# Kernel tuning notes

Measured on AMD Instinct MI355X. Metric: run time of the kernel, lower is better.

Reference implementation:

```python
import jax, jax.numpy as jnp
import numpy as np

B, N, D = 2, 2048, 256
H = 8
HD = D // H
SCALE = HD ** 0.5  # NOTE: source MULTIPLIES by sqrt(head_dim)
EPS = 1e-5
DFF = 4 * D


def setup_inputs() -> dict:
    key = jax.random.key(0)
    ks = jax.random.split(key, 9)
    s = lambda fan_in: 1.0 / np.sqrt(fan_in)
    return {
        "x": jax.random.normal(ks[0], (B, N, D), dtype=jnp.float32),
        # weights stored [in, out] (transposed torch Linear)
        "qkv_w": jax.random.normal(ks[1], (D, 3 * D), dtype=jnp.float32) * s(D),
        "proj_w": jax.random.normal(ks[2], (D, D), dtype=jnp.float32) * s(D),
        "proj_b": jax.random.normal(ks[3], (D,), dtype=jnp.float32) * 0.01,
        "fc1_w": jax.random.normal(ks[4], (D, DFF), dtype=jnp.float32) * s(D),
        "fc1_b": jax.random.normal(ks[5], (DFF,), dtype=jnp.float32) * 0.01,
        "fc2_w": jax.random.normal(ks[6], (DFF, D), dtype=jnp.float32) * s(DFF),
        "fc2_b": jax.random.normal(ks[7], (D,), dtype=jnp.float32) * 0.01,
        "ln1_g": jnp.ones((D,), dtype=jnp.float32),
        "ln1_b": jnp.zeros((D,), dtype=jnp.float32),
    }


def _layernorm(x, g, b):
    mu = jnp.mean(x, axis=-1, keepdims=True)
    var = jnp.mean(jnp.square(x - mu), axis=-1, keepdims=True)
    return (x - mu) * jax.lax.rsqrt(var + EPS) * g + b


def reference(x, qkv_w, proj_w, proj_b, fc1_w, fc1_b, fc2_w, fc2_b, ln1_g, ln1_b):
    b, n, d = x.shape
    # --- MHA ---
    qkv = (x @ qkv_w).reshape(b, n, 3, H, HD)
    q = qkv[:, :, 0].transpose(0, 2, 1, 3)  # [B,H,N,HD]
    k = qkv[:, :, 1].transpose(0, 2, 1, 3)
    v = qkv[:, :, 2].transpose(0, 2, 1, 3)
    att = jnp.einsum("bhqd,bhkd->bhqk", q, k) * SCALE  # multiplied, per source
    att = jax.nn.softmax(att, axis=-1)
    out = jnp.einsum("bhqk,bhkd->bhqd", att, v)
    out = out.transpose(0, 2, 1, 3).reshape(b, n, d)
    out = out @ proj_w + proj_b
    # --- post-norm residual ---
    net = _layernorm(out + x, ln1_g, ln1_b)
    shortcut = net
    # --- MLP (NO activation in source forward) ---
    net = (net @ fc1_w + fc1_b) @ fc2_w + fc2_b
    return net + shortcut
```

## Files before the change

### kernel.cpp

```cpp
#include <hip/hip_runtime.h>


typedef __attribute__((ext_vector_type(8))) short short8;
typedef __attribute__((ext_vector_type(4))) short bf16x4;
typedef __attribute__((ext_vector_type(4))) float floatx4;
typedef unsigned short u16;

#define MFMA32(a,b,c) __builtin_amdgcn_mfma_f32_16x16x32_bf16((a),(b),(c),0,0,0)
#if __has_builtin(__builtin_amdgcn_mfma_f32_16x16x16_bf16)
#define MFMAPV(a,b,c) __builtin_amdgcn_mfma_f32_16x16x16_bf16((a),(b),(c),0,0,0)
#else
#define MFMAPV(a,b,c) __builtin_amdgcn_mfma_f32_16x16x16bf16_1k((a),(b),(c),0,0,0)
#endif
#define CLF 8.1615404f

__device__ __forceinline__ float bf2f(u16 u) { return __uint_as_float(((unsigned)u) << 16); }
__device__ __forceinline__ u16 f2bf(float f) {
  unsigned u = __float_as_uint(f);
  u += 0x7fffu + ((u >> 16) & 1u);
  return (u16)(u >> 16);
}
__device__ __forceinline__ void gll16(const void* g, void* l) {
  __builtin_amdgcn_global_load_lds((const __attribute__((address_space(1))) void*)g,
                                   (__attribute__((address_space(3))) void*)l, 16, 0, 0);
}

__global__ __launch_bounds__(256) void prep_k(
    const void* __restrict__ x, const void* __restrict__ qkv_w,
    const void* __restrict__ proj_w, const void* __restrict__ fc1_w,
    const void* __restrict__ fc2_w, const void* __restrict__ proj_b,
    const void* __restrict__ fc1_b, const void* __restrict__ fc2_b,
    const void* __restrict__ ln_g, const void* __restrict__ ln_b,
    u16* __restrict__ x_hi, u16* __restrict__ x_lo,
    u16* __restrict__ wq_hi, u16* __restrict__ wq_lo,
    u16* __restrict__ wt_proj, u16* __restrict__ wt_fc1, u16* __restrict__ wt_fc2,
    u16* __restrict__ b_proj, u16* __restrict__ b_fc1, u16* __restrict__ b_fc2,
    u16* __restrict__ g_ln, u16* __restrict__ bb_ln)
{
  const int lane = threadIdx.x & 63;
  const float probe = bf2f(((const u16*)qkv_w)[lane]);
  const bool f32 = __ballot(!(fabsf(probe) < 1000.0f)) != 0ull;
  const int bid = blockIdx.x, tid = threadIdx.x;
  #define RD(p, i) (f32 ? ((const float*)(p))[i] : bf2f(((const u16*)(p))[i]))
  if (bid < 4096) {
    const size_t i = (size_t)bid * 256 + tid;
    const float f = RD(x, i); const u16 h = f2bf(f);
    x_hi[i] = h; x_lo[i] = f2bf(f - bf2f(h));
  } else if (bid < 4864) {
    const int idx = (bid - 4096) * 256 + tid;
    const int n = idx >> 8, k = idx & 255;
    const float f = RD(qkv_w, (size_t)k * 768 + n); const u16 h = f2bf(f);
    wq_hi[idx] = h; wq_lo[idx] = f2bf(f - bf2f(h));
  } else if (bid < 5120) {
    const int idx = (bid - 4864) * 256 + tid;
    wt_proj[idx] = f2bf(RD(proj_w, (size_t)(idx & 255) * 256 + (idx >> 8)));
  } else if (bid < 6144) {
    const int idx = (bid - 5120) * 256 + tid;
    wt_fc1[idx] = f2bf(RD(fc1_w, (size_t)(idx & 255) * 1024 + (idx >> 8)));
  } else if (bid < 7168) {
    const int idx = (bid - 6144) * 256 + tid;
    wt_fc2[idx] = f2bf(RD(fc2_w, (size_t)(idx & 1023) * 256 + (idx >> 10)));
  } else {
    const int j = (bid - 7168) * 256 + tid;
    if (j < 256)       b_proj[j]        = f2bf(RD(proj_b, j));
    else if (j < 1280) b_fc1[j - 256]   = f2bf(RD(fc1_b, j - 256));
    else if (j < 1536) b_fc2[j - 1280]  = f2bf(RD(fc2_b, j - 1280));
    else if (j < 1792) g_ln[j - 1536]   = f2bf(RD(ln_g, j - 1536));
    else               bb_ln[j - 1792]  = f2bf(RD(ln_b, j - 1792));
  }
  #undef RD
}

template<int TW, int EPI, bool BIAS, bool RES, bool SPLIT>
__global__ __launch_bounds__(256) void gemm_k(
    const u16* __restrict__ A, const u16* __restrict__ Bt,
    const u16* __restrict__ A2, const u16* __restrict__ B2,
    const u16* __restrict__ bias, const u16* __restrict__ res,
    void* __restrict__ out0, u16* __restrict__ aux1, u16* __restrict__ aux2,
    u16* __restrict__ aux3, u16* __restrict__ aux4,
    int M, int Nn, int K)
{
  constexpr int BT = TW * 32;
  constexpr int NC = (TW > 1 ? TW / 2 : 1);
  __shared__ __align__(16) short As[BT][40];
  __shared__ __align__(16) short Bs[BT][40];
  __shared__ __align__(16) short As2[SPLIT ? BT : 1][40];
  __shared__ __align__(16) short Bs2[SPLIT ? BT : 1][40];
  const int tid = threadIdx.x;
  const int m0 = blockIdx.y * BT, n0 = blockIdx.x * BT;
  const bool sp = SPLIT && (n0 < 512);
  const int wid = tid >> 6, lane = tid & 63;
  const int wm = (wid >> 1) * (TW * 16), wn = (wid & 1) * (TW * 16);
  const int lm = lane & 15, quad = lane >> 4;

  floatx4 zero = {0.f, 0.f, 0.f, 0.f};
  floatx4 acc[TW][TW];
#pragma unroll
  for (int i = 0; i < TW; ++i)
#pragma unroll
    for (int j = 0; j < TW; ++j) acc[i][j] = zero;

  int srow[NC], soff[NC];
  short8 ra[NC], rb[NC], ra2[NC], rb2[NC];
#pragma unroll
  for (int c = 0; c < NC; ++c) {
    const int cid = tid * NC + c;
    srow[c] = cid >> 2; soff[c] = (cid & 3) * 8;
  }
#pragma unroll
  for (int c = 0; c < NC; ++c) {
    const size_t ga = (size_t)(m0 + srow[c]) * K + soff[c];
    const size_t gb = (size_t)(n0 + srow[c]) * K + soff[c];
    ra[c] = *(const short8*)&A[ga];  rb[c] = *(const short8*)&Bt[gb];
    if (sp) { ra2[c] = *(const short8*)&A2[ga]; rb2[c] = *(const short8*)&B2[gb]; }
  }

  for (int k0 = 0; k0 < K; k0 += 32) {
    if (k0) __syncthreads();
#pragma unroll
    for (int c = 0; c < NC; ++c) {
      *(short8*)&As[srow[c]][soff[c]] = ra[c];
      *(short8*)&Bs[srow[c]][soff[c]] = rb[c];
      if (sp) {
        *(short8*)&As2[srow[c]][soff[c]] = ra2[c];
        *(short8*)&Bs2[srow[c]][soff[c]] = rb2[c];
      }
    }
    __syncthreads();
    if (k0 + 32 < K) {
#pragma unroll
      for (int c = 0; c < NC; ++c) {
        const size_t ga = (size_t)(m0 + srow[c]) * K + k0 + 32 + soff[c];
        const size_t gb = (size_t)(n0 + srow[c]) * K + k0 + 32 + soff[c];
        ra[c] = *(const short8*)&A[ga];  rb[c] = *(const short8*)&Bt[gb];
        if (sp) { ra2[c] = *(const short8*)&A2[ga]; rb2[c] = *(const short8*)&B2[gb]; }
      }
    }
    short8 fa[TW], fb[TW], fa2[TW], fb2[TW];
#pragma unroll
    for (int t = 0; t < TW; ++t) {
      fa[t] = *(const short8*)&As[wm + t * 16 + lm][quad * 8];
      fb[t] = *(const short8*)&Bs[wn + t * 16 + lm][quad * 8];
      if (sp) {
        fa2[t] = *(const short8*)&As2[wm + t * 16 + lm][quad * 8];
        fb2[t] = *(const short8*)&Bs2[wn + t * 16 + lm][quad * 8];
      }
    }
#pragma unroll
    for (int i = 0; i < TW; ++i)
#pragma unroll
      for (int j = 0; j < TW; ++j) {
        if (sp) {
          acc[i][j] = MFMA32(fa[i], fb2[j], acc[i][j]);
          acc[i][j] = MFMA32(fa2[i], fb[j], acc[i][j]);
        }
        acc[i][j] = MFMA32(fa[i], fb[j], acc[i][j]);
      }
  }

#pragma unroll
  for (int i = 0; i < TW; ++i) {
    const int rowb = m0 + wm + i * 16 + quad * 4;
#pragma unroll
    for (int j = 0; j < TW; ++j) {
      const int col = n0 + wn + j * 16 + lm;
      const float bv = BIAS ? bf2f(bias[col]) : 0.f;
#pragma unroll
      for (int r = 0; r < 4; ++r) {
        const int row = rowb + r;
        float v = acc[i][j][r] + bv;
        const size_t o = (size_t)row * Nn + col;
        if (RES) v += bf2f(res[o]);
        if (EPI == 0) {
          ((float*)out0)[o] = v;
        } else if (EPI == 1) {
          ((u16*)out0)[o] = f2bf(v);
        } else {
          u16 hi = f2bf(v);
          u16 lo = f2bf(v - bf2f(hi));
          if (col < 256) {
            const size_t oq = (size_t)row * 256 + col;
            aux1[oq] = hi; aux2[oq] = lo;
          } else if (col < 512) {
            const size_t ok = (size_t)row * 256 + (col - 256);
            aux3[ok] = hi; aux4[ok] = lo;
          } else {
            int d = col & 31, hh = (col >> 5) & 7;
            int bb = row >> 11, n = row & 2047;
            ((u16*)out0)[(size_t)((bb * 8 + hh) * 32 + d) * 2048 + n] = hi;
          }
        }
      }
    }
  }
}

template<int CHUNKS>
__global__ __launch_bounds__(256) void attn_k(
    const u16* __restrict__ qhi, const u16* __restrict__ qlo,
    const u16* __restrict__ khi, const u16* __restrict__ klo,
    const u16* __restrict__ vt, u16* __restrict__ outp, u16* __restrict__ out23,
    float* __restrict__ mu)
{
  __shared__ __align__(16) u16 Khi[2][64][32];
  __shared__ __align__(16) u16 Klo[2][64][32];
  __shared__ __align__(16) u16 Vs [2][32][64];
  const int tid = threadIdx.x, wid = tid >> 6, lane = tid & 63;
  const int lm = lane & 15, quad = lane >> 4;
  const int bid = blockIdx.x;
  const int chunk = (CHUNKS > 1) ? (bid >> 9) : 0;
  const int qblk = bid & 31, bh = (bid >> 5) & 15;
  const int b = bh >> 3, h = bh & 7;
  const int q0 = qblk * 64 + wid * 16;
  const size_t tb = (size_t)b * 2048;
  const int NT = 32 / CHUNKS;
  const int kofs = chunk * (2048 / CHUNKS);

  short8 qh, ql;
  { size_t off = (tb + q0 + lm) * 256 + h * 32 + quad * 8;
    qh = *(const short8*)&qhi[off];
    ql = *(const short8*)&qlo[off]; }

  const int kkey = tid >> 2, kg = tid & 3;
  const size_t kb = (tb + kofs + kkey) * 256 + h * 32 + kg * 8;
  const int vd = tid >> 3, vp = tid & 7, vk8 = vp ^ (vd & 7);
  const size_t vb = (size_t)(bh * 32 + vd) * 2048 + kofs + vk8 * 8;

  gll16(khi + kb, (u16*)Khi + tid * 8);
  gll16(klo + kb, (u16*)Klo + tid * 8);
  gll16(vt  + vb, (u16*)Vs  + tid * 8);

  float mrun = -1e30f, lrun = 0.f;
  floatx4 o0 = {0.f,0.f,0.f,0.f}, o1 = {0.f,0.f,0.f,0.f};

  for (int kt = 0; kt < NT; ++kt) {
    const int buf = kt & 1;
    __syncthreads();
    if (kt < NT - 1) {
      const int nb = (buf ^ 1) * 2048;
      const size_t ko = (size_t)(kt + 1) * 16384;
      const size_t vo = (size_t)(kt + 1) * 64;
      gll16(khi + kb + ko, (u16*)Khi + nb + tid * 8);
      gll16(klo + kb + ko, (u16*)Klo + nb + tid * 8);
      gll16(vt  + vb + vo, (u16*)Vs  + nb + tid * 8);
    }

    floatx4 z[4];
#pragma unroll
    for (int kf = 0; kf < 4; ++kf) {
      short8 khf = *(const short8*)&Khi[buf][kf * 16 + lm][quad * 8];
      short8 klf = *(const short8*)&Klo[buf][kf * 16 + lm][quad * 8];
      floatx4 zz = {0.f,0.f,0.f,0.f};
      zz = MFMA32(khf, ql, zz);
      zz = MFMA32(klf, qh, zz);
      zz = MFMA32(khf, qh, zz);
      z[kf] = zz;
    }
    float zm = fmaxf(fmaxf(fmaxf(z[0][0], z[0][1]), fmaxf(z[0][2], z[0][3])),
               fmaxf(fmaxf(z[1][0], z[1][1]), fmaxf(z[1][2], z[1][3])));
    zm = fmaxf(zm, fmaxf(fmaxf(fmaxf(z[2][0], z[2][1]), fmaxf(z[2][2], z[2][3])),
                   fmaxf(fmaxf(z[3][0], z[3][1]), fmaxf(z[3][2], z[3][3]))));
    zm = fmaxf(zm, __shfl_xor(zm, 16));
    zm = fmaxf(zm, __shfl_xor(zm, 32));
    const float mn = fmaxf(mrun, zm);
    const float alpha = exp2f((mrun - mn) * CLF);
    const float mc = mn * CLF;
    mrun = mn;
    float ls = 0.f;
    bf16x4 pb[4];
#pragma unroll
    for (int kf = 0; kf < 4; ++kf)
#pragma unroll
      for (int r = 0; r < 4; ++r) {
        const float p = exp2f(__builtin_fmaf(z[kf][r], CLF, -mc));
        ls += p;
        pb[kf][r] = (short)f2bf(p);
      }
    ls += __shfl_xor(ls, 16);
    ls += __shfl_xor(ls, 32);
    lrun = lrun * alpha + ls;
#pragma unroll
    for (int r = 0; r < 4; ++r) { o0[r] *= alpha; o1[r] *= alpha; }
    const u16* vbase = (const u16*)Vs + buf * 2048;
#pragma unroll
    for (int kf = 0; kf < 4; ++kf) {
      const int k8 = 2 * kf + (quad >> 1);
      const int d0 = lm, d1 = 16 + lm;
      bf16x4 vf0 = *(const bf16x4*)(vbase + (d0 * 8 + (k8 ^ (d0 & 7))) * 8 + (quad & 1) * 4);
      bf16x4 vf1 = *(const bf16x4*)(vbase + (d1 * 8 + (k8 ^ (d1 & 7))) * 8 + (quad & 1) * 4);
      o0 = MFMAPV(vf0, pb[kf], o0);
      o1 = MFMAPV(vf1, pb[kf], o1);
    }
  }
  const float inv = 1.0f / lrun;
  const size_t tok = tb + q0 + lm;
  u16* dst = ((CHUNKS > 2 && chunk >= 2) ? out23 : outp) + (size_t)(chunk & 1) * 1048576;
  const size_t rowo = tok * 256 + h * 32;
#pragma unroll
  for (int r = 0; r < 4; ++r) {
    dst[rowo + quad * 4 + r]      = f2bf(o0[r] * inv);
    dst[rowo + 16 + quad * 4 + r] = f2bf(o1[r] * inv);
  }
  if (CHUNKS > 1 && quad == 0)
    mu[chunk * 32768 + tok * 8 + h] = __builtin_fmaf(mrun, CLF, __log2f(lrun));
}

template<int CHUNKS>
__global__ __launch_bounds__(256) void combine_k(u16* __restrict__ d,
                                                 const u16* __restrict__ e,
                                                 const float* __restrict__ mu)
{
  const int t = blockIdx.x, c = threadIdx.x, h = c >> 5;
  const size_t o = (size_t)t * 256 + c;
  float m[CHUNKS];
  float M = -1e30f;
#pragma unroll
  for (int i = 0; i < CHUNKS; ++i) { m[i] = mu[i * 32768 + t * 8 + h]; M = fmaxf(M, m[i]); }
  float wsum = 0.f, acc = 0.f;
#pragma unroll
  for (int i = 0; i < CHUNKS; ++i) {
    const float w = exp2f(m[i] - M);
    const u16 v = (i < 2) ? d[o + (size_t)i * 1048576] : e[o + (size_t)(i - 2) * 1048576];
    wsum += w; acc += w * bf2f(v);
  }
  d[o] = f2bf(acc / wsum);
}

__global__ __launch_bounds__(256) void ln_k(const float* __restrict__ pf,
                                            const u16* __restrict__ xh,
                                            const u16* __restrict__ xl,
                                            const u16* __restrict__ g,
                                            const u16* __restrict__ bta,
                                            u16* __restrict__ net)
{
  const int t = blockIdx.x, c = threadIdx.x;
  const size_t o = (size_t)t * 256 + c;
  float v = pf[o] + bf2f(xh[o]) + bf2f(xl[o]);
  float s = v, s2 = v * v;
#pragma unroll
  for (int d = 1; d < 64; d <<= 1) { s += __shfl_xor(s, d); s2 += __shfl_xor(s2, d); }
  __shared__ float ss[4], ss2[4];
  const int w = c >> 6;
  if ((c & 63) == 0) { ss[w] = s; ss2[w] = s2; }
  __syncthreads();
  s = ss[0] + ss[1] + ss[2] + ss[3];
  s2 = ss2[0] + ss2[1] + ss2[2] + ss2[3];
  const float mu = s * (1.f / 256.f);
  const float var = s2 * (1.f / 256.f) - mu * mu;
  const float is = rsqrtf(var + 1e-5f);
  net[o] = f2bf((v - mu) * is * bf2f(g[c]) + bf2f(bta[c]));
}

extern "C" void kernel_launch(void* const* d_in, const int* in_sizes, int n_in,
                              void* d_out, int out_size, void* d_ws, size_t ws_size,
                              hipStream_t stream) {
  const void* x      = d_in[0];
  const void* qkv_w  = d_in[1];
  const void* proj_w = d_in[2];
  const void* proj_b = d_in[3];
  const void* fc1_w  = d_in[4];
  const void* fc1_b  = d_in[5];
  const void* fc2_w  = d_in[6];
  const void* fc2_b  = d_in[7];
  const void* ln_g   = d_in[8];
  const void* ln_b   = d_in[9];

  char* ws = (char*)d_ws;
  u16* b_proj  = (u16*)(ws + 4096);
  u16* b_fc1   = (u16*)(ws + 8192);
  u16* b_fc2   = (u16*)(ws + 12288);
  u16* g_ln    = (u16*)(ws + 16384);
  u16* bb_ln   = (u16*)(ws + 20480);
  u16* wq_hi   = (u16*)(ws + 131072);
  u16* wq_lo   = (u16*)(ws + 524288);
  u16* wt_proj = (u16*)(ws + 917504);
  u16* wt_fc1  = (u16*)(ws + 1048576);
  u16* wt_fc2  = (u16*)(ws + 1572864);
  u16* x_hi    = (u16*)(ws + 2097152);
  u16* x_lo    = (u16*)(ws + 4194304);
  u16* q_hi    = (u16*)(ws + 6291456);
  u16* q_lo    = (u16*)(ws + 8388608);
  u16* k_hi    = (u16*)(ws + 10485760);
  u16* k_lo    = (u16*)(ws + 12582912);
  u16* vt      = (u16*)(ws + 14680064);
  float* mu    = (float*)(ws + 16777216);
  u16* out23   = (u16*)(ws + 17301504);
  u16* attn    = (u16*)d_out;
  float* projf = (float*)(ws + 6291456);
  u16* net     = (u16*)(ws + 14680064);
  u16* hbuf    = (u16*)(ws + 2097152);

  const bool sk4 = ws_size >= (17301504 + 4194304);
  const bool sk2 = ws_size >= (16777216 + 262144);

  prep_k<<<7176, 256, 0, stream>>>(x, qkv_w, proj_w, fc1_w, fc2_w,
                                   proj_b, fc1_b, fc2_b, ln_g, ln_b,
                                   x_hi, x_lo, wq_hi, wq_lo, wt_proj, wt_fc1, wt_fc2,
                                   b_proj, b_fc1, b_fc2, g_ln, bb_ln);

  gemm_k<2, 2, false, false, true><<<dim3(12, 64), 256, 0, stream>>>(
      x_hi, wq_hi, x_lo, wq_lo, nullptr, nullptr, vt, q_hi, q_lo, k_hi, k_lo, 4096, 768, 256);
  if (sk4) {
    attn_k<4><<<2048, 256, 0, stream>>>(q_hi, q_lo, k_hi, k_lo, vt, attn, out23, mu);
    combine_k<4><<<4096, 256, 0, stream>>>(attn, out23, mu);
  } else if (sk2) {
    attn_k<2><<<1024, 256, 0, stream>>>(q_hi, q_lo, k_hi, k_lo, vt, attn, nullptr, mu);
    combine_k<2><<<4096, 256, 0, stream>>>(attn, nullptr, mu);
  } else {
    attn_k<1><<<512, 256, 0, stream>>>(q_hi, q_lo, k_hi, k_lo, vt, attn, nullptr, nullptr);
  }
  gemm_k<2, 0, true, false, false><<<dim3(4, 64), 256, 0, stream>>>(
      attn, wt_proj, nullptr, nullptr, b_proj, nullptr, projf,
      nullptr, nullptr, nullptr, nullptr, 4096, 256, 256);
  ln_k<<<4096, 256, 0, stream>>>(projf, x_hi, x_lo, g_ln, bb_ln, net);
  gemm_k<2, 1, true, false, false><<<dim3(16, 64), 256, 0, stream>>>(
      net, wt_fc1, nullptr, nullptr, b_fc1, nullptr, hbuf,
      nullptr, nullptr, nullptr, nullptr, 4096, 1024, 256);
  gemm_k<2, 0, true, true, false><<<dim3(4, 64), 256, 0, stream>>>(
      hbuf, wt_fc2, nullptr, nullptr, b_fc2, net, d_out,
      nullptr, nullptr, nullptr, nullptr, 4096, 256, 1024);
}
```

Baseline: 169.5 us.

## Fuse split-KV combine into proj GEMM and coalesce V-transpose stores via LDS

After: 163.7 us. 3.5% less time.

```diff
diff --git a/kernel.cpp b/kernel.cpp
--- a/kernel.cpp
+++ b/kernel.cpp
@@ -4,6 +4,7 @@
 typedef __attribute__((ext_vector_type(8))) short short8;
 typedef __attribute__((ext_vector_type(4))) short bf16x4;
 typedef __attribute__((ext_vector_type(4))) float floatx4;
+typedef __attribute__((ext_vector_type(2))) unsigned int uint2v;
 typedef unsigned short u16;
 
 #define MFMA32(a,b,c) __builtin_amdgcn_mfma_f32_16x16x32_bf16((a),(b),(c),0,0,0)
@@ -14,11 +15,25 @@
 #endif
 #define CLF 8.1615404f
 
+#if __has_builtin(__builtin_amdgcn_exp2f)
+#define EX2(x) __builtin_amdgcn_exp2f(x)
+#else
+#define EX2(x) exp2f(x)
+#endif
+
 __device__ __forceinline__ float bf2f(u16 u) { return __uint_as_float(((unsigned)u) << 16); }
 __device__ __forceinline__ u16 f2bf(float f) {
   unsigned u = __float_as_uint(f);
   u += 0x7fffu + ((u >> 16) & 1u);
   return (u16)(u >> 16);
+}
+__device__ __forceinline__ unsigned pkbf2(float a, float b) {
+#if __has_builtin(__builtin_amdgcn_perm)
+  return __builtin_amdgcn_perm(__float_as_uint(b) + 0x8000u,
+                               __float_as_uint(a) + 0x8000u, 0x07060302u);
+#else
+  return (unsigned)f2bf(a) | ((unsigned)f2bf(b) << 16);
+#endif
 }
 __device__ __forceinline__ void gll16(const void* g, void* l) {
   __builtin_amdgcn_global_load_lds((const __attribute__((address_space(1))) void*)g,
@@ -71,13 +86,13 @@
   #undef RD
 }
 
-template<int TW, int EPI, bool BIAS, bool RES, bool SPLIT>
+template<int TW, int EPI, bool BIAS, bool RES, bool SPLIT, bool COMB>
 __global__ __launch_bounds__(256) void gemm_k(
     const u16* __restrict__ A, const u16* __restrict__ Bt,
     const u16* __restrict__ A2, const u16* __restrict__ B2,
     const u16* __restrict__ bias, const u16* __restrict__ res,
     void* __restrict__ out0, u16* __restrict__ aux1, u16* __restrict__ aux2,
-    u16* __restrict__ aux3, u16* __restrict__ aux4,
+    u16* __restrict__ aux3, u16* __restrict__ aux4, const float* __restrict__ muc,
     int M, int Nn, int K)
 {
   constexpr int BT = TW * 32;
@@ -86,6 +101,7 @@
   __shared__ __align__(16) short Bs[BT][40];
   __shared__ __align__(16) short As2[SPLIT ? BT : 1][40];
   __shared__ __align__(16) short Bs2[SPLIT ? BT : 1][40];
+  __shared__ __align__(16) u16 Vt[(EPI == 2) ? 64 * 72 : 1];
   const int tid = threadIdx.x;
   const int m0 = blockIdx.y * BT, n0 = blockIdx.x * BT;
   const bool sp = SPLIT && (n0 < 512);
@@ -101,18 +117,45 @@
     for (int j = 0; j < TW; ++j) acc[i][j] = zero;
 
   int srow[NC], soff[NC];
-  short8 ra[NC], rb[NC], ra2[NC], rb2[NC];
 #pragma unroll
   for (int c = 0; c < NC; ++c) {
     const int cid = tid * NC + c;
     srow[c] = cid >> 2; soff[c] = (cid & 3) * 8;
   }
+
+  auto comb8 = [&](int t, int col8) -> short8 {
+    const size_t o = (size_t)t * 256 + col8;
+    const int h = col8 >> 5;
+    const float m0_ = muc[t * 8 + h],          m1_ = muc[32768 + t * 8 + h];
+    const float m2_ = muc[65536 + t * 8 + h],  m3_ = muc[98304 + t * 8 + h];
+    const float M = fmaxf(fmaxf(m0_, m1_), fmaxf(m2_, m3_));
+    float w0 = EX2(m0_ - M), w1 = EX2(m1_ - M), w2 = EX2(m2_ - M), w3 = EX2(m3_ - M);
+    const float inv = 1.f / (w0 + w1 + w2 + w3);
+    w0 *= inv; w1 *= inv; w2 *= inv; w3 *= inv;
+    short8 a0 = *(const short8*)&A[o],  a1 = *(const short8*)&A[o + 1048576];
+    short8 a2 = *(const short8*)&A2[o], a3 = *(const short8*)&A2[o + 1048576];
+    float v[8];
+#pragma unroll
+    for (int j = 0; j < 8; ++j)
+      v[j] = w0 * bf2f(a0[j]) + w1 * bf2f(a1[j]) + w2 * bf2f(a2[j]) + w3 * bf2f(a3[j]);
+    uint2v uu0 = {pkbf2(v[0], v[1]), pkbf2(v[2], v[3])};
+    uint2v uu1 = {pkbf2(v[4], v[5]), pkbf2(v[6], v[7])};
+    short8 r;
+    *(uint2v*)&r = uu0; *((uint2v*)&r + 1) = uu1;
+    return r;
+  };
+
+  short8 ra[NC], rb[NC], ra2[NC], rb2[NC];
 #pragma unroll
   for (int c = 0; c < NC; ++c) {
-    const size_t ga = (size_t)(m0 + srow[c]) * K + soff[c];
     const size_t gb = (size_t)(n0 + srow[c]) * K + soff[c];
-    ra[c] = *(const short8*)&A[ga];  rb[c] = *(const short8*)&Bt[gb];
-    if (sp) { ra2[c] = *(const short8*)&A2[ga]; rb2[c] = *(const short8*)&B2[gb]; }
+    rb[c] = *(const short8*)&Bt[gb];
+    if (COMB) ra[c] = comb8(m0 + srow[c], soff[c]);
+    else      ra[c] = *(const short8*)&A[(size_t)(m0 + srow[c]) * K + soff[c]];
+    if (sp) {
+      ra2[c] = *(const short8*)&A2[(size_t)(m0 + srow[c]) * K + soff[c]];
+      rb2[c] = *(const short8*)&B2[gb];
+    }
   }
 
   for (int k0 = 0; k0 < K; k0 += 32) {
@@ -130,10 +173,14 @@
     if (k0 + 32 < K) {
 #pragma unroll
       for (int c = 0; c < NC; ++c) {
-        const size_t ga = (size_t)(m0 + srow[c]) * K + k0 + 32 + soff[c];
         const size_t gb = (size_t)(n0 + srow[c]) * K + k0 + 32 + soff[c];
-        ra[c] = *(const short8*)&A[ga];  rb[c] = *(const short8*)&Bt[gb];
-        if (sp) { ra2[c] = *(const short8*)&A2[ga]; rb2[c] = *(const short8*)&B2[gb]; }
+        rb[c] = *(const short8*)&Bt[gb];
+        if (COMB) ra[c] = comb8(m0 + srow[c], k0 + 32 + soff[c]);
+        else      ra[c] = *(const short8*)&A[(size_t)(m0 + srow[c]) * K + k0 + 32 + soff[c]];
+        if (sp) {
+          ra2[c] = *(const short8*)&A2[(size_t)(m0 + srow[c]) * K + k0 + 32 + soff[c]];
+          rb2[c] = *(const short8*)&B2[gb];
+        }
       }
     }
     short8 fa[TW], fb[TW], fa2[TW], fb2[TW];
@@ -156,6 +203,29 @@
         }
         acc[i][j] = MFMA32(fa[i], fb[j], acc[i][j]);
       }
+  }
+
+  if (EPI == 2 && n0 >= 512) {
+    __syncthreads();
+#pragma unroll
+    for (int i = 0; i < TW; ++i)
+#pragma unroll
+      for (int j = 0; j < TW; ++j)
+#pragma unroll
+        for (int r = 0; r < 4; ++r)
+          Vt[(wn + j * 16 + lm) * 72 + wm + i * 16 + quad * 4 + r] = f2bf(acc[i][j][r]);
+    __syncthreads();
+    const int bb = m0 >> 11, n = m0 & 2047;
+#pragma unroll
+    for (int pass = 0; pass < 2; ++pass) {
+      const int dl = (tid >> 3) + pass * 32;
+      const int oct = tid & 7;
+      const int col = n0 - 512 + dl;
+      const int d = col & 31, hh = col >> 5;
+      short8 v = *(const short8*)&Vt[dl * 72 + oct * 8];
+      *(short8*)&((u16*)out0)[(size_t)((bb * 8 + hh) * 32 + d) * 2048 + n + oct * 8] = v;
+    }
+    return;
   }
 
 #pragma unroll
@@ -181,13 +251,9 @@
           if (col < 256) {
             const size_t oq = (size_t)row * 256 + col;
             aux1[oq] = hi; aux2[oq] = lo;
-          } else if (col < 512) {
+          } else {
             const size_t ok = (size_t)row * 256 + (col - 256);
             aux3[ok] = hi; aux4[ok] = lo;
-          } else {
-            int d = col & 31, hh = (col >> 5) & 7;
-            int bb = row >> 11, n = row & 2047;
-            ((u16*)out0)[(size_t)((bb * 8 + hh) * 32 + d) * 2048 + n] = hi;
           }
         }
       }
@@ -263,19 +329,21 @@
     zm = fmaxf(zm, __shfl_xor(zm, 16));
     zm = fmaxf(zm, __shfl_xor(zm, 32));
     const float mn = fmaxf(mrun, zm);
-    const float alpha = exp2f((mrun - mn) * CLF);
+    const float alpha = EX2((mrun - mn) * CLF);
     const float mc = mn * CLF;
     mrun = mn;
     float ls = 0.f;
     bf16x4 pb[4];
 #pragma unroll
-    for (int kf = 0; kf < 4; ++kf)
-#pragma unroll
-      for (int r = 0; r < 4; ++r) {
-        const float p = exp2f(__builtin_fmaf(z[kf][r], CLF, -mc));
-        ls += p;
-        pb[kf][r] = (short)f2bf(p);
-      }
+    for (int kf = 0; kf < 4; ++kf) {
+      const float p0 = EX2(__builtin_fmaf(z[kf][0], CLF, -mc));
+      const float p1 = EX2(__builtin_fmaf(z[kf][1], CLF, -mc));
+      const float p2 = EX2(__builtin_fmaf(z[kf][2], CLF, -mc));
+      const float p3 = EX2(__builtin_fmaf(z[kf][3], CLF, -mc));
+      ls += (p0 + p1) + (p2 + p3);
+      uint2v uu = {pkbf2(p0, p1), pkbf2(p2, p3)};
+      pb[kf] = *(bf16x4*)&uu;
+    }
     ls += __shfl_xor(ls, 16);
     ls += __shfl_xor(ls, 32);
     lrun = lrun * alpha + ls;
@@ -319,7 +387,7 @@
   float wsum = 0.f, acc = 0.f;
 #pragma unroll
   for (int i = 0; i < CHUNKS; ++i) {
-    const float w = exp2f(m[i] - M);
+    const float w = EX2(m[i] - M);
     const u16 v = (i < 2) ? d[o + (size_t)i * 1048576] : e[o + (size_t)(i - 2) * 1048576];
     wsum += w; acc += w * bf2f(v);
   }
@@ -398,25 +466,31 @@
                                    x_hi, x_lo, wq_hi, wq_lo, wt_proj, wt_fc1, wt_fc2,
                                    b_proj, b_fc1, b_fc2, g_ln, bb_ln);
 
-  gemm_k<2, 2, false, false, true><<<dim3(12, 64), 256, 0, stream>>>(
-      x_hi, wq_hi, x_lo, wq_lo, nullptr, nullptr, vt, q_hi, q_lo, k_hi, k_lo, 4096, 768, 256);
+  gemm_k<2, 2, false, false, true, false><<<dim3(12, 64), 256, 0, stream>>>(
+      x_hi, wq_hi, x_lo, wq_lo, nullptr, nullptr, vt, q_hi, q_lo, k_hi, k_lo,
+      nullptr, 4096, 768, 256);
   if (sk4) {
     attn_k<4><<<2048, 256, 0, stream>>>(q_hi, q_lo, k_hi, k_lo, vt, attn, out23, mu);
-    combine_k<4><<<4096, 256, 0, stream>>>(attn, out23, mu);
+    gemm_k<2, 0, true, false, false, true><<<dim3(4, 64), 256, 0, stream>>>(
+        attn, wt_proj, out23, nullptr, b_proj, nullptr, projf,
+        nullptr, nullptr, nullptr, nullptr, mu, 4096, 256, 256);
   } else if (sk2) {
     attn_k<2><<<1024, 256, 0, stream>>>(q_hi, q_lo, k_hi, k_lo, vt, attn, nullptr, mu);
     combine_k<2><<<4096, 256, 0, stream>>>(attn, nullptr, mu);
+    gemm_k<2, 0, true, false, false, false><<<dim3(4, 64), 256, 0, stream>>>(
+        attn, wt_proj, nullptr, nullptr, b_proj, nullptr, projf,
+        nullptr, nullptr, nullptr, nullptr, nullptr, 4096, 256, 256);
   } else {
     attn_k<1><<<512, 256, 0, stream>>>(q_hi, q_lo, k_hi, k_lo, vt, attn, nullptr, nullptr);
-  }
-  gemm_k<2, 0, true, false, false><<<dim3(4, 64), 256, 0, stream>>>(
-      attn, wt_proj, nullptr, nullptr, b_proj, nullptr, projf,
-      nullptr, nullptr, nullptr, nullptr, 4096, 256, 256);
+    gemm_k<2, 0, true, false, false, false><<<dim3(4, 64), 256, 0, stream>>>(
+        attn, wt_proj, nullptr, nullptr, b_proj, nullptr, projf,
+        nullptr, nullptr, nullptr, nullptr, nullptr, 4096, 256, 256);
+  }
   ln_k<<<4096, 256, 0, stream>>>(projf, x_hi, x_lo, g_ln, bb_ln, net);
-  gemm_k<2, 1, true, false, false><<<dim3(16, 64), 256, 0, stream>>>(
+  gemm_k<2, 1, true, false, false, false><<<dim3(16, 64), 256, 0, stream>>>(
       net, wt_fc1, nullptr, nullptr, b_fc1, nullptr, hbuf,
-      nullptr, nullptr, nullptr, nullptr, 4096, 1024, 256);
-  gemm_k<2, 0, true, true, false><<<dim3(4, 64), 256, 0, stream>>>(
+      nullptr, nullptr, nullptr, nullptr, nullptr, 4096, 1024, 256);
+  gemm_k<2, 0, true, true, false, false><<<dim3(4, 64), 256, 0, stream>>>(
       hbuf, wt_fc2, nullptr, nullptr, b_fc2, net, d_out,
-      nullptr, nullptr, nullptr, nullptr, 4096, 256, 1024);
-}
+      nullptr, nullptr, nullptr, nullptr, nullptr, 4096, 256, 1024);
+}
```
